# Kernel tuning notes

Measured on AMD Instinct MI355X. Metric: run time of the kernel, lower is better.

## Reference

```python
import jax, jax.numpy as jnp
import numpy as np

B, S, E, M = 128, 196, 768, 768

def setup_inputs() -> dict:
    key = jax.random.key(0)
    k1, k2, k3, k4, k5 = jax.random.split(key, 5)
    sent_emb = jax.random.normal(k1, (B, S, E), dtype=jnp.float32)
    # valid event spans: start in [0, S-6), end = start + len, len in [1,5]
    starts = jax.random.randint(k2, (B, 2), 0, S - 6)
    lens = jax.random.randint(k3, (B, 2), 1, 6)
    ends = starts + lens
    batch_e = jnp.stack([starts[:, 0], ends[:, 0], starts[:, 1], ends[:, 1]], axis=1).astype(jnp.int64)
    mlp_w = jax.random.normal(k4, (M, 2 * E), dtype=jnp.float32) * 0.02
    mlp_b = jnp.zeros((M,), dtype=jnp.float32)
    fk_w = jax.random.normal(k5, (M, S * E), dtype=jnp.float32) * 0.005
    fk_b = jnp.zeros((M,), dtype=jnp.float32)
    return {"sent_emb": sent_emb, "batch_e": batch_e, "mlp_w": mlp_w,
            "mlp_b": mlp_b, "fk_w": fk_w, "fk_b": fk_b, "batch_size": B}

def reference(sent_emb, batch_e, mlp_w, mlp_b, fk_w, fk_b, batch_size):
    b, s, e = sent_emb.shape
    # sent_process: flatten each sentence's [S,E] embeddings into one row [S*E]
    sent_emb_cat = sent_emb.reshape(b, s * e)  # [B, S*E]
    # extract_event: mean-pool over the two variable-length spans (vectorized via masks)
    pos = jnp.arange(s)  # [S]
    m1 = ((pos >= batch_e[:, 0:1]) & (pos < batch_e[:, 1:2])).astype(sent_emb.dtype)  # [B,S]
    m2 = ((pos >= batch_e[:, 2:3]) & (pos < batch_e[:, 3:4])).astype(sent_emb.dtype)
    e1 = jnp.einsum('bs,bse->be', m1, sent_emb) / jnp.sum(m1, axis=1, keepdims=True)
    e2 = jnp.einsum('bs,bse->be', m2, sent_emb) / jnp.sum(m2, axis=1, keepdims=True)
    event_pair = jnp.concatenate([e1, e2], axis=1)  # [B, 2E]
    pred = 0.9 * (event_pair @ mlp_w.T + mlp_b) + 0.1 * (sent_emb_cat @ fk_w.T + fk_b)
    return pred
```

## Files before the change

### kernel.cpp

```cpp
#include <hip/hip_runtime.h>
#include <hip/hip_bf16.h>

#define B_ 128
#define S_ 196
#define E_ 768
#define M_ 768
#define KTOT (S_*E_)
#define SUPER 64
#define NT 96
#define KSPLIT 96
#define ZC 4

typedef __bf16 bf16x8 __attribute__((ext_vector_type(8)));
typedef __bf16 bf16x4 __attribute__((ext_vector_type(4)));
typedef float  f32x4  __attribute__((ext_vector_type(4)));

__device__ inline bf16x8 cvt8(const float* __restrict__ p) {
    float4 a = *(const float4*)p;
    float4 b = *(const float4*)(p + 4);
    bf16x8 r;
    r[0] = (__bf16)a.x; r[1] = (__bf16)a.y; r[2] = (__bf16)a.z; r[3] = (__bf16)a.w;
    r[4] = (__bf16)b.x; r[5] = (__bf16)b.y; r[6] = (__bf16)b.z; r[7] = (__bf16)b.w;
    return r;
}

__global__ void init_out(const float* __restrict__ mlp_b,
                         const float* __restrict__ fk_b,
                         float* __restrict__ out) {
    int i = blockIdx.x * 256 + threadIdx.x;
    if (i < B_ * M_) {
        int m = i % M_;
        out[i] = 0.9f * mlp_b[m] + 0.1f * fk_b[m];
    }
}

__global__ void cvt_a(const float* __restrict__ A, __bf16* __restrict__ Abf) {
    const int n8 = (B_ * KTOT) / 8;
    for (int i = blockIdx.x * blockDim.x + threadIdx.x; i < n8;
         i += gridDim.x * blockDim.x) {
        *(bf16x8*)(Abf + (size_t)i * 8) = cvt8(A + (size_t)i * 8);
    }
}

__global__ void event_pool(const float* __restrict__ SE,
                           const int* __restrict__ BE, int be_stride,
                           float* __restrict__ EP) {
    int b = blockIdx.x;
    int s1 = BE[(b*4 + 0) * be_stride];
    int e1 = BE[(b*4 + 1) * be_stride];
    int s2 = BE[(b*4 + 2) * be_stride];
    int e2 = BE[(b*4 + 3) * be_stride];
    float inv1 = 1.0f / (float)(e1 - s1);
    float inv2 = 1.0f / (float)(e2 - s2);
    for (int c = threadIdx.x; c < E_; c += 256) {
        float sum1 = 0.f, sum2 = 0.f;
        for (int s = s1; s < e1; ++s) sum1 += SE[((size_t)b * S_ + s) * E_ + c];
        for (int s = s2; s < e2; ++s) sum2 += SE[((size_t)b * S_ + s) * E_ + c];
        EP[b * (2*E_) + c]       = sum1 * inv1;
        EP[b * (2*E_) + E_ + c]  = sum2 * inv2;
    }
}

__global__ __launch_bounds__(256) void mlp_gemm(const float* __restrict__ EP,
                                                const float* __restrict__ Wm,
                                                float* __restrict__ out) {
    const int wid   = (blockIdx.x * 256 + threadIdx.x) >> 6;
    const int lane  = threadIdx.x & 63;
    const int bt    = wid & 7;
    const int mt    = wid >> 3;
    const int row16 = lane & 15;
    const int kgrp  = lane >> 4;
    const float* Arow = EP + (size_t)(bt*16 + row16) * (2*E_);
    const float* Brow = Wm + (size_t)(mt*16 + row16) * (2*E_);
    f32x4 acc = {};
    for (int k0 = 0; k0 < 2*E_; k0 += 32) {
        bf16x8 af = cvt8(Arow + k0 + kgrp*8);
        bf16x8 bv = cvt8(Brow + k0 + kgrp*8);
        acc = __builtin_amdgcn_mfma_f32_16x16x32_bf16(af, bv, acc, 0, 0, 0);
    }
    const int m = mt*16 + row16;
#pragma unroll
    for (int r = 0; r < 4; ++r) {
        const int b = bt*16 + kgrp*4 + r;
        out[b * M_ + m] += 0.9f * acc[r];
    }
}

__global__ __launch_bounds__(512) void fk_gemm(const __bf16* __restrict__ Abf,
                                               const float* __restrict__ W,
                                               float* __restrict__ partial) {
    __shared__ __align__(16) char Wlds[2][NT * 128];

    const int wgid = blockIdx.x;
    const int xcd  = wgid & 7;
    const int slot = wgid >> 3;
    const int kz   = xcd + 8 * (slot >> 3);
    const int mt   = slot & 7;

    const int ss_total = KTOT / SUPER;
    const int ss0 = (ss_total * kz) / KSPLIT;
    const int ss1 = (ss_total * (kz + 1)) / KSPLIT;

    const int tid   = threadIdx.x;
    const int wave  = tid >> 6;
    const int lane  = tid & 63;
    const int row16 = lane & 15;
    const int kgrp  = lane >> 4;

    const float* wp[3];
    int wbyte[3];
#pragma unroll
    for (int i = 0; i < 3; ++i) {
        int fid = tid + i * 512;
        int r = fid >> 4, cq = fid & 15;
        wp[i]    = W + (size_t)(mt * NT + r) * KTOT + cq * 4;
        wbyte[i] = r * 128 + ((cq * 8) ^ ((r & 7) << 4));
    }

    const __bf16* Arow = Abf + (size_t)(wave * 16 + row16) * KTOT;
    const int swz = (row16 & 7) << 4;

    f32x4 acc[6] = {};
    float4 v[3];

#pragma unroll
    for (int i = 0; i < 3; ++i) v[i] = *(const float4*)(wp[i] + ss0 * SUPER);
#pragma unroll
    for (int i = 0; i < 3; ++i) {
        bf16x4 h;
        h[0] = (__bf16)v[i].x; h[1] = (__bf16)v[i].y;
        h[2] = (__bf16)v[i].z; h[3] = (__bf16)v[i].w;
        *(bf16x4*)(&Wlds[0][0] + wbyte[i]) = h;
    }
    __syncthreads();

    for (int ss = ss0; ss < ss1; ++ss) {
        const int buf = (ss - ss0) & 1;
        const int k0 = ss * SUPER;
        const bool more = (ss + 1 < ss1);

        if (more) {
#pragma unroll
            for (int i = 0; i < 3; ++i) v[i] = *(const float4*)(wp[i] + k0 + SUPER);
        }

        bf16x8 af0 = *(const bf16x8*)(Arow + k0 + kgrp * 8);
        bf16x8 af1 = *(const bf16x8*)(Arow + k0 + 32 + kgrp * 8);

        const char* Wb = &Wlds[buf][0];
#pragma unroll
        for (int n = 0; n < 6; ++n) {
            bf16x8 wf = *(const bf16x8*)(Wb + (n * 16 + row16) * 128 + ((kgrp * 16) ^ swz));
            acc[n] = __builtin_amdgcn_mfma_f32_16x16x32_bf16(af0, wf, acc[n], 0, 0, 0);
        }
#pragma unroll
        for (int n = 0; n < 6; ++n) {
            bf16x8 wf = *(const bf16x8*)(Wb + (n * 16 + row16) * 128 + ((64 + kgrp * 16) ^ swz));
            acc[n] = __builtin_amdgcn_mfma_f32_16x16x32_bf16(af1, wf, acc[n], 0, 0, 0);
        }

        if (more) {
#pragma unroll
            for (int i = 0; i < 3; ++i) {
                bf16x4 h;
                h[0] = (__bf16)v[i].x; h[1] = (__bf16)v[i].y;
                h[2] = (__bf16)v[i].z; h[3] = (__bf16)v[i].w;
                *(bf16x4*)(&Wlds[buf ^ 1][0] + wbyte[i]) = h;
            }
        }
        __syncthreads();
    }

    float* pz = partial + (size_t)kz * (B_ * M_);
#pragma unroll
    for (int n = 0; n < 6; ++n) {
        const int m = mt * NT + n * 16 + row16;
#pragma unroll
        for (int r = 0; r < 4; ++r) {
            const int b = wave * 16 + kgrp * 4 + r;
            pz[(size_t)b * M_ + m] = acc[n][r];
        }
    }
}

__global__ void reduce_k(const float* __restrict__ pp, float* __restrict__ out) {
    int t = blockIdx.x * 256 + threadIdx.x;
    int i = t % (B_ * M_);
    int zc = t / (B_ * M_);
    if (zc >= ZC) return;
    float s = 0.f;
#pragma unroll
    for (int z = zc * (KSPLIT / ZC); z < (zc + 1) * (KSPLIT / ZC); ++z)
        s += pp[(size_t)z * (B_ * M_) + i];
    atomicAdd(out + i, 0.1f * s);
}

extern "C" void kernel_launch(void* const* d_in, const int* in_sizes, int n_in,
                              void* d_out, int out_size, void* d_ws, size_t ws_size,
                              hipStream_t stream) {
    const float* se    = (const float*)d_in[0];
    const int*   be    = (const int*)  d_in[1];
    const float* mlp_w = (const float*)d_in[2];
    const float* mlp_b = (const float*)d_in[3];
    const float* fk_w  = (const float*)d_in[4];
    const float* fk_b  = (const float*)d_in[5];
    float* out = (float*)d_out;
    float* ep  = (float*)d_ws;
    float* pp  = ep + (size_t)B_ * 2 * E_;
    __bf16* abf = (__bf16*)(pp + (size_t)KSPLIT * B_ * M_);

    const int be_stride = (in_sizes[1] == B_ * 4 * 2) ? 2 : 1;

    init_out<<<(B_ * M_ + 255) / 256, 256, 0, stream>>>(mlp_b, fk_b, out);
    cvt_a<<<2048, 256, 0, stream>>>(se, abf);
    event_pool<<<B_, 256, 0, stream>>>(se, be, be_stride, ep);
    mlp_gemm<<<(B_ / 16) * (M_ / 16) / 4, 256, 0, stream>>>(ep, mlp_w, out);
    fk_gemm<<<8 * KSPLIT, 512, 0, stream>>>(abf, fk_w, pp);
    reduce_k<<<(B_ * M_ * ZC + 255) / 256, 256, 0, stream>>>(pp, out);
}
```

Baseline: 190.2 us.

## Restructure fk GEMM to register-streamed weights without LDS, fewer K splits

The fk GEMM now gives each wave a 16-column M tile across all 128 batch rows. Weight fragments are streamed straight from global memory into registers and converted to bf16 there, replacing the LDS double-buffered weight tile and its per-step barriers. The K split drops from 96 to 32, so each wave runs a longer 147-step loop and the partial-sum buffer that reduce_k reads is smaller. In exchange, every wave re-reads the bf16 activation rows for all 128 batches, which multiplies activation traffic across M tiles. The grid is also much smaller, leaving few waves per CU to hide memory latency.

```diff
diff --git a/kernel.cpp b/kernel.cpp
--- a/kernel.cpp
+++ b/kernel.cpp
@@ -6,18 +6,23 @@
 #define E_ 768
 #define M_ 768
 #define KTOT (S_*E_)
-#define SUPER 64
-#define NT 96
-#define KSPLIT 96
+#define KSPLIT 32
+#define STEPS 147
 #define ZC 4
 
 typedef __bf16 bf16x8 __attribute__((ext_vector_type(8)));
-typedef __bf16 bf16x4 __attribute__((ext_vector_type(4)));
 typedef float  f32x4  __attribute__((ext_vector_type(4)));
 
 __device__ inline bf16x8 cvt8(const float* __restrict__ p) {
     float4 a = *(const float4*)p;
     float4 b = *(const float4*)(p + 4);
+    bf16x8 r;
+    r[0] = (__bf16)a.x; r[1] = (__bf16)a.y; r[2] = (__bf16)a.z; r[3] = (__bf16)a.w;
+    r[4] = (__bf16)b.x; r[5] = (__bf16)b.y; r[6] = (__bf16)b.z; r[7] = (__bf16)b.w;
+    return r;
+}
+
+__device__ inline bf16x8 cvt8v(float4 a, float4 b) {
     bf16x8 r;
     r[0] = (__bf16)a.x; r[1] = (__bf16)a.y; r[2] = (__bf16)a.z; r[3] = (__bf16)a.w;
     r[4] = (__bf16)b.x; r[5] = (__bf16)b.y; r[6] = (__bf16)b.z; r[7] = (__bf16)b.w;
@@ -86,99 +91,69 @@
     }
 }
 
-__global__ __launch_bounds__(512) void fk_gemm(const __bf16* __restrict__ Abf,
+__global__ __launch_bounds__(256) void fk_gemm(const __bf16* __restrict__ Abf,
                                                const float* __restrict__ W,
                                                float* __restrict__ partial) {
-    __shared__ __align__(16) char Wlds[2][NT * 128];
-
     const int wgid = blockIdx.x;
     const int xcd  = wgid & 7;
     const int slot = wgid >> 3;
-    const int kz   = xcd + 8 * (slot >> 3);
-    const int mt   = slot & 7;
-
-    const int ss_total = KTOT / SUPER;
-    const int ss0 = (ss_total * kz) / KSPLIT;
-    const int ss1 = (ss_total * (kz + 1)) / KSPLIT;
-
-    const int tid   = threadIdx.x;
-    const int wave  = tid >> 6;
-    const int lane  = tid & 63;
+    const int kzg  = slot / 12;
+    const int wsl  = slot % 12;
+    const int kz   = xcd + 8 * kzg;
+    const int wave = threadIdx.x >> 6;
+    const int mt   = wsl * 4 + wave;
+    const int lane  = threadIdx.x & 63;
     const int row16 = lane & 15;
     const int kgrp  = lane >> 4;
 
-    const float* wp[3];
-    int wbyte[3];
+    const int kbase = kz * (STEPS * 32);
+    const float*  wbase = W   + (size_t)(mt * 16 + row16) * KTOT + kbase + kgrp * 8;
+    const __bf16* abase = Abf + (size_t)row16 * KTOT + kbase + kgrp * 8;
+
+    f32x4 acc[8] = {};
+    float4 wn0, wn1;
+    bf16x8 an[8];
+
+    wn0 = *(const float4*)(wbase);
+    wn1 = *(const float4*)(wbase + 4);
 #pragma unroll
-    for (int i = 0; i < 3; ++i) {
-        int fid = tid + i * 512;
-        int r = fid >> 4, cq = fid & 15;
-        wp[i]    = W + (size_t)(mt * NT + r) * KTOT + cq * 4;
-        wbyte[i] = r * 128 + ((cq * 8) ^ ((r & 7) << 4));
+    for (int bt = 0; bt < 8; ++bt)
+        an[bt] = *(const bf16x8*)(abase + (size_t)bt * 16 * KTOT);
+
+    for (int s = 0; s < STEPS - 1; ++s) {
+        float4 wc0 = wn0, wc1 = wn1;
+        bf16x8 ac[8];
+#pragma unroll
+        for (int bt = 0; bt < 8; ++bt) ac[bt] = an[bt];
+
+        const float*  wp = wbase + (s + 1) * 32;
+        const __bf16* ap = abase + (s + 1) * 32;
+        wn0 = *(const float4*)(wp);
+        wn1 = *(const float4*)(wp + 4);
+#pragma unroll
+        for (int bt = 0; bt < 8; ++bt)
+            an[bt] = *(const bf16x8*)(ap + (size_t)bt * 16 * KTOT);
+
+        bf16x8 wf = cvt8v(wc0, wc1);
+#pragma unroll
+        for (int bt = 0; bt < 8; ++bt)
+            acc[bt] = __builtin_amdgcn_mfma_f32_16x16x32_bf16(ac[bt], wf, acc[bt], 0, 0, 0);
     }
-
-    const __bf16* Arow = Abf + (size_t)(wave * 16 + row16) * KTOT;
-    const int swz = (row16 & 7) << 4;
-
-    f32x4 acc[6] = {};
-    float4 v[3];
-
+    {
+        bf16x8 wf = cvt8v(wn0, wn1);
 #pragma unroll
-    for (int i = 0; i < 3; ++i) v[i] = *(const float4*)(wp[i] + ss0 * SUPER);
-#pragma unroll
-    for (int i = 0; i < 3; ++i) {
-        bf16x4 h;
-        h[0] = (__bf16)v[i].x; h[1] = (__bf16)v[i].y;
-        h[2] = (__bf16)v[i].z; h[3] = (__bf16)v[i].w;
-        *(bf16x4*)(&Wlds[0][0] + wbyte[i]) = h;
-    }
-    __syncthreads();
-
-    for (int ss = ss0; ss < ss1; ++ss) {
-        const int buf = (ss - ss0) & 1;
-        const int k0 = ss * SUPER;
-        const bool more = (ss + 1 < ss1);
-
-        if (more) {
-#pragma unroll
-            for (int i = 0; i < 3; ++i) v[i] = *(const float4*)(wp[i] + k0 + SUPER);
-        }
-
-        bf16x8 af0 = *(const bf16x8*)(Arow + k0 + kgrp * 8);
-        bf16x8 af1 = *(const bf16x8*)(Arow + k0 + 32 + kgrp * 8);
-
-        const char* Wb = &Wlds[buf][0];
-#pragma unroll
-        for (int n = 0; n < 6; ++n) {
-            bf16x8 wf = *(const bf16x8*)(Wb + (n * 16 + row16) * 128 + ((kgrp * 16) ^ swz));
-            acc[n] = __builtin_amdgcn_mfma_f32_16x16x32_bf16(af0, wf, acc[n], 0, 0, 0);
-        }
-#pragma unroll
-        for (int n = 0; n < 6; ++n) {
-            bf16x8 wf = *(const bf16x8*)(Wb + (n * 16 + row16) * 128 + ((64 + kgrp * 16) ^ swz));
-            acc[n] = __builtin_amdgcn_mfma_f32_16x16x32_bf16(af1, wf, acc[n], 0, 0, 0);
-        }
-
-        if (more) {
-#pragma unroll
-            for (int i = 0; i < 3; ++i) {
-                bf16x4 h;
-                h[0] = (__bf16)v[i].x; h[1] = (__bf16)v[i].y;
-                h[2] = (__bf16)v[i].z; h[3] = (__bf16)v[i].w;
-                *(bf16x4*)(&Wlds[buf ^ 1][0] + wbyte[i]) = h;
-            }
-        }
-        __syncthreads();
+        for (int bt = 0; bt < 8; ++bt)
+            acc[bt] = __builtin_amdgcn_mfma_f32_16x16x32_bf16(an[bt], wf, acc[bt], 0, 0, 0);
     }
 
     float* pz = partial + (size_t)kz * (B_ * M_);
+    const int m = mt * 16 + row16;
 #pragma unroll
-    for (int n = 0; n < 6; ++n) {
-        const int m = mt * NT + n * 16 + row16;
+    for (int bt = 0; bt < 8; ++bt) {
 #pragma unroll
         for (int r = 0; r < 4; ++r) {
-            const int b = wave * 16 + kgrp * 4 + r;
-            pz[(size_t)b * M_ + m] = acc[n][r];
+            const int b = bt * 16 + kgrp * 4 + r;
+            pz[(size_t)b * M_ + m] = acc[bt][r];
         }
     }
 }
@@ -215,6 +190,6 @@
     cvt_a<<<2048, 256, 0, stream>>>(se, abf);
     event_pool<<<B_, 256, 0, stream>>>(se, be, be_stride, ep);
     mlp_gemm<<<(B_ / 16) * (M_ / 16) / 4, 256, 0, stream>>>(ep, mlp_w, out);
-    fk_gemm<<<8 * KSPLIT, 512, 0, stream>>>(abf, fk_w, pp);
+    fk_gemm<<<(M_ / 16) * KSPLIT / 4, 256, 0, stream>>>(abf, fk_w, pp);
     reduce_k<<<(B_ * M_ * ZC + 255) / 256, 256, 0, stream>>>(pp, out);
 }
```

Result: slower. 451.3 us, median of 2 (+137.3%).
